# Kernel optimization log

Hardware: AMD Instinct MI355X
Metric: run time of the kernel (lower is better)

Reference implementation:

```python
import jax, jax.numpy as jnp
import numpy as np

B, S, E, H, F = 8, 1024, 1024, 16, 4096
HD = E // H
EPS = 1e-12
NEG = -1e30  # stands in for -inf on fully-masked key positions


def layernorm(x, w, b):
    mu = jnp.mean(x, axis=-1, keepdims=True)
    var = jnp.mean(jnp.square(x - mu), axis=-1, keepdims=True)
    return (x - mu) * jax.lax.rsqrt(var + EPS) * w + b


def setup_inputs() -> dict:
    key = jax.random.key(0)
    ks = jax.random.split(key, 12)
    s = 0.02
    return {
        "final_hidden_state": jax.random.normal(ks[0], (B, S, E), jnp.float32),
        "attention_mask": jax.random.randint(ks[1], (B, S), 0, 2, jnp.int64),
        "token_type_ids": jax.random.randint(ks[2], (B, S), 0, 2, jnp.int64),
        # MultiheadAttention in/out projections (stored input-major: [in, out])
        "in_proj_w": jax.random.normal(ks[3], (E, 3 * E), jnp.float32) * s,
        "in_proj_b": jnp.zeros((3 * E,), jnp.float32),
        "out_proj_w": jax.random.normal(ks[4], (E, E), jnp.float32) * s,
        "out_proj_b": jnp.zeros((E,), jnp.float32),
        # shared LayerNorm
        "ln_w": jnp.ones((E,), jnp.float32),
        "ln_b": jnp.zeros((E,), jnp.float32),
        # FFN
        "w_in": jax.random.normal(ks[5], (E, F), jnp.float32) * s,
        "b_in": jnp.zeros((F,), jnp.float32),
        "w_out": jax.random.normal(ks[6], (F, E), jnp.float32) * s,
        "b_out": jnp.zeros((E,), jnp.float32),
    }


def reference(final_hidden_state, attention_mask, token_type_ids,
              in_proj_w, in_proj_b, out_proj_w, out_proj_b,
              ln_w, ln_b, w_in, b_in, w_out, b_out):
    x = final_hidden_state  # [B,S,E]
    am = attention_mask != 0
    # key_padding_mask: True = ignore this key; first position always masked
    question_mask = (token_type_ids == 1) | (~am)
    question_mask = question_mask.at[:, 0].set(True)  # [B,S]
    # float attn_mask ADDED to scores (PyTorch adds float attn_mask): pairwise 0/1
    amf = (am[:, :, None] & am[:, None, :]).astype(x.dtype)  # [B,S,S]

    # qkv projections
    qkv = x @ in_proj_w + in_proj_b  # [B,S,3E]
    q, k, v = jnp.split(qkv, 3, axis=-1)
    q = q.reshape(B, S, H, HD)
    k = k.reshape(B, S, H, HD)
    v = v.reshape(B, S, H, HD)

    scores = jnp.einsum("bqhd,bkhd->bhqk", q, k) / np.sqrt(HD)
    scores = scores + amf[:, None, :, :]  # additive float mask (0/1!)
    scores = jnp.where(question_mask[:, None, None, :], NEG, scores)
    probs = jax.nn.softmax(scores, axis=-1)

    ctx = jnp.einsum("bhqk,bkhd->bqhd", probs, v).reshape(B, S, E)
    attn_out = ctx @ out_proj_w + out_proj_b

    h = layernorm(attn_out + x, ln_w, ln_b)
    ff = jax.nn.gelu(h @ w_in + b_in, approximate=False) @ w_out + b_out
    return layernorm(ff + h, ln_w, ln_b)
```

## Files before the change

### kernel.cpp

```cpp
#include <hip/hip_runtime.h>
#include <hip/hip_bf16.h>
#include <math.h>

#define B_ 8
#define S_ 1024
#define E_ 1024
#define H_ 16
#define HD_ 64
#define F_ 4096
#define M_ (B_ * S_)

typedef float f32x4 __attribute__((ext_vector_type(4)));
typedef short short8 __attribute__((ext_vector_type(8)));

__device__ inline unsigned short f2bf(float x) {
    union { float f; unsigned int u; } v; v.f = x;
    unsigned int r = (v.u + 0x7fffu + ((v.u >> 16) & 1u)) >> 16;
    return (unsigned short)r;
}
__device__ inline float bf2f(unsigned short u) {
    union { unsigned int u; float f; } v; v.u = ((unsigned int)u) << 16;
    return v.f;
}

__device__ inline float erf_inline(float x) {
    float ax = __builtin_fabsf(x);
    float t = __builtin_amdgcn_rcpf(1.0f + 0.3275911f * ax);
    float y = t * (0.254829592f + t * (-0.284496736f + t * (1.421413741f +
              t * (-1.453152027f + t * 1.061405429f))));
    float e = __expf(-ax * ax);
    float r = 1.0f - y * e;
    union { float f; unsigned int u; } s, o;
    s.f = x; o.f = r;
    o.u = (o.u & 0x7fffffffu) | (s.u & 0x80000000u);
    return o.f;
}

#define AS1 __attribute__((address_space(1)))
#define AS3 __attribute__((address_space(3)))
__device__ inline void gload_lds16(const void* g, void* l) {
    __builtin_amdgcn_global_load_lds((const AS1 unsigned int*)(g),
                                     (AS3 unsigned int*)(l), 16, 0, 0);
}

__global__ __launch_bounds__(256) void cast_f32_bf16(const float* __restrict__ in,
                                                     unsigned short* __restrict__ out) {
    int i = (blockIdx.x * 256 + threadIdx.x) * 4;
    float4 v = *(const float4*)(in + i);
    ushort4 o;
    o.x = f2bf(v.x); o.y = f2bf(v.y); o.z = f2bf(v.z); o.w = f2bf(v.w);
    *(ushort4*)(out + i) = o;
}

__global__ __launch_bounds__(256) void mask_prep(const int* __restrict__ am,
                                                 const int* __restrict__ tt,
                                                 float* __restrict__ amqf,
                                                 float* __restrict__ negadd) {
    int i = blockIdx.x * 256 + threadIdx.x;
    int s = i & (S_ - 1);
    int a = am[i], t = tt[i];
    amqf[i] = (a != 0) ? 1.0f : 0.0f;
    negadd[i] = ((t == 1) || (a == 0) || (s == 0)) ? -1e30f : 0.0f;
}

__global__ __launch_bounds__(256) void transpose_cast(const float* __restrict__ in,
                                                      unsigned short* __restrict__ out,
                                                      int K, int N) {
    __shared__ float tile[32][33];
    int n0 = blockIdx.x * 32, k0 = blockIdx.y * 32;
    int tc = threadIdx.x & 31, tr = threadIdx.x >> 5;
    for (int i = 0; i < 4; ++i) {
        int k = k0 + tr + i * 8;
        tile[tr + i * 8][tc] = in[(size_t)k * N + n0 + tc];
    }
    __syncthreads();
    for (int i = 0; i < 4; ++i) {
        int n = n0 + tr + i * 8;
        out[(size_t)n * K + k0 + tc] = f2bf(tile[tc][tr + i * 8]);
    }
}

#define BM 128
#define BN 128
#define BK 32
template <int EPI>
__global__ __launch_bounds__(256) void gemm_bt(const unsigned short* __restrict__ A,
                                               const unsigned short* __restrict__ Bt,
                                               const float* __restrict__ bias,
                                               const float* __restrict__ res,
                                               unsigned short* __restrict__ Cb,
                                               float* __restrict__ Cf,
                                               int M, int N, int K) {
    __shared__ unsigned short lA[BM * BK];
    __shared__ unsigned short lB[BN * BK];
    int row0 = blockIdx.y * BM, col0 = blockIdx.x * BN;
    int t = threadIdx.x;
    int lane = t & 63, w = t >> 6;
    int wr = w >> 1, wc = w & 1;
    int qa = lane >> 4, ml = lane & 15;

    f32x4 acc[4][4] = {};
    const unsigned short* Aptr = A + (size_t)row0 * K;
    const unsigned short* Bptr = Bt + (size_t)col0 * K;

    for (int k0 = 0; k0 < K; k0 += BK) {
        __syncthreads();
        for (int i = 0; i < 2; ++i) {
            int c = t + i * 256;
            int r = c >> 2, kc = c & 3;
            gload_lds16(Aptr + (size_t)r * K + k0 + kc * 8, lA + c * 8);
            gload_lds16(Bptr + (size_t)r * K + k0 + kc * 8, lB + c * 8);
        }
        __syncthreads();
        short8 af[4], bfr[4];
        for (int i = 0; i < 4; ++i)
            af[i] = *(const short8*)&lA[(wr * 64 + i * 16 + ml) * BK + qa * 8];
        for (int j = 0; j < 4; ++j)
            bfr[j] = *(const short8*)&lB[(wc * 64 + j * 16 + ml) * BK + qa * 8];
        for (int i = 0; i < 4; ++i)
            for (int j = 0; j < 4; ++j)
                acc[i][j] = __builtin_amdgcn_mfma_f32_16x16x32_bf16(af[i], bfr[j], acc[i][j], 0, 0, 0);
    }

    for (int i = 0; i < 4; ++i) {
        for (int j = 0; j < 4; ++j) {
            int col = col0 + wc * 64 + j * 16 + ml;
            float bv = bias[col];
            for (int r = 0; r < 4; ++r) {
                int row = row0 + wr * 64 + i * 16 + qa * 4 + r;
                float cv = acc[i][j][r] + bv;
                if (EPI == 0) {
                    if (col < 1024) cv *= 0.125f;
                    Cb[(size_t)row * N + col] = f2bf(cv);
                } else if (EPI == 1) {
                    cv = 0.5f * cv * (1.0f + erf_inline(cv * 0.70710678118654752f));
                    Cb[(size_t)row * N + col] = f2bf(cv);
                } else {
                    cv += res[(size_t)row * N + col];
                    Cf[(size_t)row * N + col] = cv;
                }
            }
        }
    }
}

__global__ __launch_bounds__(256) void transpose_v(const unsigned short* __restrict__ qkv,
                                                   unsigned short* __restrict__ vT) {
    __shared__ unsigned short tile[64][72];
    int s0 = blockIdx.x * 64;
    int pair = blockIdx.y;
    int b = pair >> 4, h = pair & 15;
    int t = threadIdx.x;
    int r = t >> 2, c0 = (t & 3) * 16;
    const unsigned short* src = qkv + (size_t)(b * S_ + s0 + r) * 3072 + 2048 + h * 64 + c0;
    *(short8*)&tile[r][c0] = *(const short8*)src;
    *(short8*)&tile[r][c0 + 8] = *(const short8*)(src + 8);
    __syncthreads();
    int d = t >> 2, sc0 = (t & 3) * 16;
    unsigned short tmp[16];
    for (int i = 0; i < 16; ++i) tmp[i] = tile[sc0 + i][d];
    unsigned short* dst = vT + ((size_t)pair * 64 + d) * S_ + s0 + sc0;
    *(short8*)dst = *(const short8*)&tmp[0];
    *(short8*)(dst + 8) = *(const short8*)&tmp[8];
}

__global__ __launch_bounds__(256) void attn_flash(const unsigned short* __restrict__ qkv,
                                                  const unsigned short* __restrict__ vT,
                                                  const float* __restrict__ amqf,
                                                  const float* __restrict__ negadd,
                                                  unsigned short* __restrict__ ctx) {
    __shared__ unsigned short lK[128 * 64];
    __shared__ unsigned short lP[4][16 * 136];
    int qc = blockIdx.x;
    int pair = blockIdx.y;
    int b = pair >> 4, h = pair & 15;
    int t = threadIdx.x, w = t >> 6, lane = t & 63;
    int qa = lane >> 4, ml = lane & 15;
    int q0 = qc * 64 + w * 16;

    const unsigned short* qrow = qkv + (size_t)(b * S_ + q0 + ml) * 3072 + h * 64;
    short8 aq0 = *(const short8*)(qrow + qa * 8);
    short8 aq1 = *(const short8*)(qrow + 32 + qa * 8);
    float amq[4];
    for (int r = 0; r < 4; ++r) amq[r] = amqf[b * S_ + q0 + qa * 4 + r];

    const unsigned short* ksrc[4];
    unsigned short* kdst[4];
    for (int i = 0; i < 4; ++i) {
        int c = w * 256 + i * 64 + lane;
        int row = c >> 3, slot = c & 7, e8 = slot ^ (row & 7);
        ksrc[i] = qkv + (size_t)(b * S_ + row) * 3072 + 1024 + h * 64 + e8 * 8;
        kdst[i] = lK + c * 8;
    }
    int sw0 = qa ^ (ml & 7);
    int sw1 = (qa + 4) ^ (ml & 7);

    float m_old[4] = {-3e38f, -3e38f, -3e38f, -3e38f};
    float l[4] = {0.f, 0.f, 0.f, 0.f};
    f32x4 O[4] = {};
    unsigned short* pw = lP[w];

    for (int kc = 0; kc < 8; ++kc) {
        int kk0 = kc * 128;
        __syncthreads();
        for (int i = 0; i < 4; ++i)
            gload_lds16(ksrc[i] + (size_t)kk0 * 3072, kdst[i]);
        __syncthreads();

        f32x4 sacc[8];
        for (int ks = 0; ks < 8; ++ks) {
            int keyoff = (ks * 16 + ml) * 64;
            short8 bb0 = *(const short8*)(lK + keyoff + sw0 * 8);
            short8 bb1 = *(const short8*)(lK + keyoff + sw1 * 8);
            f32x4 a = {};
            a = __builtin_amdgcn_mfma_f32_16x16x32_bf16(aq0, bb0, a, 0, 0, 0);
            a = __builtin_amdgcn_mfma_f32_16x16x32_bf16(aq1, bb1, a, 0, 0, 0);
            float sb = negadd[b * S_ + kk0 + ks * 16 + ml];
            for (int r = 0; r < 4; ++r) a[r] += amq[r] + sb;
            sacc[ks] = a;
        }
        float m_new[4], alpha[4], sum[4];
        for (int r = 0; r < 4; ++r) {
            float m = m_old[r];
            for (int ks = 0; ks < 8; ++ks) m = fmaxf(m, sacc[ks][r]);
            for (int o = 8; o >= 1; o >>= 1) m = fmaxf(m, __shfl_xor(m, o, 16));
            m_new[r] = m;
            alpha[r] = __expf(m_old[r] - m);
            m_old[r] = m;
            sum[r] = 0.f;
        }
        for (int ks = 0; ks < 8; ++ks) {
            for (int r = 0; r < 4; ++r) {
                float p = __expf(sacc[ks][r] - m_new[r]);
                sum[r] += p;
                pw[(qa * 4 + r) * 136 + ks * 16 + ml] = f2bf(p);
            }
        }
        for (int r = 0; r < 4; ++r) {
            float s = sum[r];
            for (int o = 8; o >= 1; o >>= 1) s += __shfl_xor(s, o, 16);
            l[r] = l[r] * alpha[r] + s;
        }
        for (int ds = 0; ds < 4; ++ds)
            for (int r = 0; r < 4; ++r)
                O[ds][r] *= alpha[r];
        for (int ds = 0; ds < 4; ++ds) {
            const unsigned short* vtp = vT + ((size_t)pair * 64 + ds * 16 + ml) * S_ + kk0;
            for (int kst = 0; kst < 4; ++kst) {
                short8 ap = *(const short8*)(pw + ml * 136 + kst * 32 + qa * 8);
                short8 bp = *(const short8*)(vtp + kst * 32 + qa * 8);
                O[ds] = __builtin_amdgcn_mfma_f32_16x16x32_bf16(ap, bp, O[ds], 0, 0, 0);
            }
        }
    }
    for (int r = 0; r < 4; ++r) {
        float inv = 1.0f / l[r];
        size_t orow = (size_t)(b * S_ + q0 + qa * 4 + r) * E_ + h * 64;
        for (int ds = 0; ds < 4; ++ds)
            ctx[orow + ds * 16 + ml] = f2bf(O[ds][r] * inv);
    }
}

template <int WRITE_BF16>
__global__ __launch_bounds__(256) void ln_kernel(const float* __restrict__ in,
                                                 const float* __restrict__ lw,
                                                 const float* __restrict__ lb,
                                                 float* __restrict__ outf,
                                                 unsigned short* __restrict__ outb) {
    int row = blockIdx.x;
    int t = threadIdx.x;
    const float* x = in + (size_t)row * E_;
    float4 v = ((const float4*)x)[t];
    float s = v.x + v.y + v.z + v.w;
    float sq = v.x * v.x + v.y * v.y + v.z * v.z + v.w * v.w;
    for (int o = 32; o >= 1; o >>= 1) {
        s += __shfl_xor(s, o, 64);
        sq += __shfl_xor(sq, o, 64);
    }
    __shared__ float red[8];
    if ((t & 63) == 0) { red[t >> 6] = s; red[4 + (t >> 6)] = sq; }
    __syncthreads();
    s = red[0] + red[1] + red[2] + red[3];
    sq = red[4] + red[5] + red[6] + red[7];
    float mu = s * (1.0f / E_);
    float var = sq * (1.0f / E_) - mu * mu;
    float rstd = rsqrtf(fmaxf(var, 0.0f) + 1e-12f);
    float4 wv = ((const float4*)lw)[t];
    float4 bv = ((const float4*)lb)[t];
    float4 o;
    o.x = (v.x - mu) * rstd * wv.x + bv.x;
    o.y = (v.y - mu) * rstd * wv.y + bv.y;
    o.z = (v.z - mu) * rstd * wv.z + bv.z;
    o.w = (v.w - mu) * rstd * wv.w + bv.w;
    ((float4*)(outf + (size_t)row * E_))[t] = o;
    if (WRITE_BF16) {
        ushort4 ob;
        ob.x = f2bf(o.x); ob.y = f2bf(o.y); ob.z = f2bf(o.z); ob.w = f2bf(o.w);
        ((ushort4*)(outb + (size_t)row * E_))[t] = ob;
    }
}

extern "C" void kernel_launch(void* const* d_in, const int* in_sizes, int n_in,
                              void* d_out, int out_size, void* d_ws, size_t ws_size,
                              hipStream_t stream) {
    const float* x        = (const float*)d_in[0];
    const int*   am       = (const int*)d_in[1];
    const int*   tt       = (const int*)d_in[2];
    const float* in_w     = (const float*)d_in[3];
    const float* in_b     = (const float*)d_in[4];
    const float* out_w    = (const float*)d_in[5];
    const float* out_b    = (const float*)d_in[6];
    const float* ln_w     = (const float*)d_in[7];
    const float* ln_b     = (const float*)d_in[8];
    const float* w_in     = (const float*)d_in[9];
    const float* b_in     = (const float*)d_in[10];
    const float* w_out    = (const float*)d_in[11];
    const float* b_out    = (const float*)d_in[12];
    float* out = (float*)d_out;

    const size_t MB = 1024 * 1024;
    char* ws = (char*)d_ws;
    unsigned short* xb    = (unsigned short*)(ws + 0);
    unsigned short* hb    = xb;
    unsigned short* wqkvT = (unsigned short*)(ws + 16 * MB);
    unsigned short* woutT = (unsigned short*)(ws + 22 * MB);
    unsigned short* winT  = (unsigned short*)(ws + 24 * MB);
    unsigned short* wo2T  = (unsigned short*)(ws + 32 * MB);
    unsigned short* qkvb  = (unsigned short*)(ws + 40 * MB);
    unsigned short* vT    = (unsigned short*)(ws + 88 * MB);
    unsigned short* ctx   = (unsigned short*)(ws + 104 * MB);
    float*          res1  = (float*)(ws + 120 * MB);
    float*          hbuf  = (float*)(ws + 152 * MB);
    unsigned short* ffmid = (unsigned short*)(ws + 184 * MB);
    float*          amqf  = (float*)(ws + 184 * MB);
    float*          negadd= (float*)(ws + 185 * MB);

    cast_f32_bf16<<<dim3(M_ * E_ / 1024), 256, 0, stream>>>(x, xb);
    mask_prep<<<dim3(M_ / 256), 256, 0, stream>>>(am, tt, amqf, negadd);
    transpose_cast<<<dim3(3 * E_ / 32, E_ / 32), 256, 0, stream>>>(in_w, wqkvT, E_, 3 * E_);
    transpose_cast<<<dim3(E_ / 32, E_ / 32), 256, 0, stream>>>(out_w, woutT, E_, E_);
    transpose_cast<<<dim3(F_ / 32, E_ / 32), 256, 0, stream>>>(w_in, winT, E_, F_);
    transpose_cast<<<dim3(E_ / 32, F_ / 32), 256, 0, stream>>>(w_out, wo2T, F_, E_);
    gemm_bt<0><<<dim3(3 * E_ / BN, M_ / BM), 256, 0, stream>>>(xb, wqkvT, in_b, nullptr,
                                                               qkvb, nullptr, M_, 3 * E_, E_);
    transpose_v<<<dim3(S_ / 64, B_ * H_), 256, 0, stream>>>(qkvb, vT);
    attn_flash<<<dim3(S_ / 64, B_ * H_), 256, 0, stream>>>(qkvb, vT, amqf, negadd, ctx);
    gemm_bt<2><<<dim3(E_ / BN, M_ / BM), 256, 0, stream>>>(ctx, woutT, out_b, x,
                                                           nullptr, res1, M_, E_, E_);
    ln_kernel<1><<<dim3(M_), 256, 0, stream>>>(res1, ln_w, ln_b, hbuf, hb);
    gemm_bt<1><<<dim3(F_ / BN, M_ / BM), 256, 0, stream>>>(hb, winT, b_in, nullptr,
                                                           ffmid, nullptr, M_, F_, E_);
    gemm_bt<2><<<dim3(E_ / BN, M_ / BM), 256, 0, stream>>>(ffmid, wo2T, b_out, hbuf,
                                                           nullptr, res1, M_, E_, F_);
    ln_kernel<0><<<dim3(M_), 256, 0, stream>>>(res1, ln_w, ln_b, out, nullptr);
}
```

Baseline: 690.7 us.

## Compute transposed S tile and keep P in registers, dropping LDS round trip

The QK^T MFMA now runs with the K and Q operands swapped, so each lane holds scores for a single query row across keys. The row max and row sum then reduce with two cross-lane shuffles instead of four per row. The P fragments are packed to bf16 with v_cvt_pk_bf16_f32 and rearranged into the PV A-operand layout through lane shuffles, removing the per-warp LDS buffer and its writes and reads. In exchange, alpha and l must be redistributed to the output layout with extra shuffles, and the permutation logic is intricate and easy to get wrong.

```diff
diff --git a/kernel.cpp b/kernel.cpp
--- a/kernel.cpp
+++ b/kernel.cpp
@@ -170,7 +170,6 @@
                                                   const float* __restrict__ negadd,
                                                   unsigned short* __restrict__ ctx) {
     __shared__ unsigned short lK[128 * 64];
-    __shared__ unsigned short lP[4][16 * 136];
     int qc = blockIdx.x;
     int pair = blockIdx.y;
     int b = pair >> 4, h = pair & 15;
@@ -179,10 +178,10 @@
     int q0 = qc * 64 + w * 16;
 
     const unsigned short* qrow = qkv + (size_t)(b * S_ + q0 + ml) * 3072 + h * 64;
-    short8 aq0 = *(const short8*)(qrow + qa * 8);
-    short8 aq1 = *(const short8*)(qrow + 32 + qa * 8);
-    float amq[4];
-    for (int r = 0; r < 4; ++r) amq[r] = amqf[b * S_ + q0 + qa * 4 + r];
+    short8 bq0 = *(const short8*)(qrow + qa * 8);
+    short8 bq1 = *(const short8*)(qrow + 32 + qa * 8);
+    float amq = amqf[b * S_ + q0 + ml];
+    const f32x4* na4 = (const f32x4*)(negadd + b * S_);
 
     const unsigned short* ksrc[4];
     unsigned short* kdst[4];
@@ -194,11 +193,14 @@
     }
     int sw0 = qa ^ (ml & 7);
     int sw1 = (qa + 4) ^ (ml & 7);
-
-    float m_old[4] = {-3e38f, -3e38f, -3e38f, -3e38f};
-    float l[4] = {0.f, 0.f, 0.f, 0.f};
+    int qa4 = qa * 4;
+    int gbase = lane & 48;
+    bool hi = lane >= 32;
+    bool odd = (qa & 1);
+
+    float m_old = -3e38f;
+    float l = 0.f;
     f32x4 O[4] = {};
-    unsigned short* pw = lP[w];
 
     for (int kc = 0; kc < 8; ++kc) {
         int kk0 = kc * 128;
@@ -210,52 +212,78 @@
         f32x4 sacc[8];
         for (int ks = 0; ks < 8; ++ks) {
             int keyoff = (ks * 16 + ml) * 64;
-            short8 bb0 = *(const short8*)(lK + keyoff + sw0 * 8);
-            short8 bb1 = *(const short8*)(lK + keyoff + sw1 * 8);
+            short8 ak0 = *(const short8*)(lK + keyoff + sw0 * 8);
+            short8 ak1 = *(const short8*)(lK + keyoff + sw1 * 8);
             f32x4 a = {};
-            a = __builtin_amdgcn_mfma_f32_16x16x32_bf16(aq0, bb0, a, 0, 0, 0);
-            a = __builtin_amdgcn_mfma_f32_16x16x32_bf16(aq1, bb1, a, 0, 0, 0);
-            float sb = negadd[b * S_ + kk0 + ks * 16 + ml];
-            for (int r = 0; r < 4; ++r) a[r] += amq[r] + sb;
+            a = __builtin_amdgcn_mfma_f32_16x16x32_bf16(ak0, bq0, a, 0, 0, 0);
+            a = __builtin_amdgcn_mfma_f32_16x16x32_bf16(ak1, bq1, a, 0, 0, 0);
+            f32x4 nb = na4[(kk0 >> 2) + ks * 4 + qa];
+            for (int r = 0; r < 4; ++r) a[r] += amq + nb[r];
             sacc[ks] = a;
         }
-        float m_new[4], alpha[4], sum[4];
-        for (int r = 0; r < 4; ++r) {
-            float m = m_old[r];
-            for (int ks = 0; ks < 8; ++ks) m = fmaxf(m, sacc[ks][r]);
-            for (int o = 8; o >= 1; o >>= 1) m = fmaxf(m, __shfl_xor(m, o, 16));
-            m_new[r] = m;
-            alpha[r] = __expf(m_old[r] - m);
-            m_old[r] = m;
-            sum[r] = 0.f;
-        }
-        for (int ks = 0; ks < 8; ++ks) {
+
+        float m = m_old;
+        for (int ks = 0; ks < 8; ++ks)
+            for (int r = 0; r < 4; ++r) m = fmaxf(m, sacc[ks][r]);
+        m = fmaxf(m, __shfl_xor(m, 16));
+        m = fmaxf(m, __shfl_xor(m, 32));
+        float m_new = m;
+        float alpha = __expf(m_old - m_new);
+        m_old = m_new;
+
+        float s_sum = 0.f;
+        short8 pfrag[4];
+        for (int kst = 0; kst < 4; ++kst) {
+            f32x4 e0, e1;
             for (int r = 0; r < 4; ++r) {
-                float p = __expf(sacc[ks][r] - m_new[r]);
-                sum[r] += p;
-                pw[(qa * 4 + r) * 136 + ks * 16 + ml] = f2bf(p);
+                e0[r] = __expf(sacc[2 * kst][r] - m_new);
+                e1[r] = __expf(sacc[2 * kst + 1][r] - m_new);
+                s_sum += e0[r] + e1[r];
             }
-        }
-        for (int r = 0; r < 4; ++r) {
-            float s = sum[r];
-            for (int o = 8; o >= 1; o >>= 1) s += __shfl_xor(s, o, 16);
-            l[r] = l[r] * alpha[r] + s;
-        }
+            unsigned int u0, u1, v0, v1;
+            asm("v_cvt_pk_bf16_f32 %0, %1, %2" : "=v"(u0) : "v"(e0[0]), "v"(e0[1]));
+            asm("v_cvt_pk_bf16_f32 %0, %1, %2" : "=v"(u1) : "v"(e0[2]), "v"(e0[3]));
+            asm("v_cvt_pk_bf16_f32 %0, %1, %2" : "=v"(v0) : "v"(e1[0]), "v"(e1[1]));
+            asm("v_cvt_pk_bf16_f32 %0, %1, %2" : "=v"(v1) : "v"(e1[2]), "v"(e1[3]));
+            unsigned int u0x = __shfl_xor(u0, 32), v0x = __shfl_xor(v0, 32);
+            unsigned int u1x = __shfl_xor(u1, 32), v1x = __shfl_xor(v1, 32);
+            unsigned int A0 = hi ? v0x : u0;
+            unsigned int B0 = hi ? v0  : u0x;
+            unsigned int A1 = hi ? v1x : u1;
+            unsigned int B1 = hi ? v1  : u1x;
+            unsigned int A0x = __shfl_xor(A0, 16), B0x = __shfl_xor(B0, 16);
+            unsigned int A1x = __shfl_xor(A1, 16), B1x = __shfl_xor(B1, 16);
+            union { short8 s8; unsigned int u[4]; } pk;
+            pk.u[0] = odd ? B0x : A0;
+            pk.u[1] = odd ? B1x : A1;
+            pk.u[2] = odd ? B0  : A0x;
+            pk.u[3] = odd ? B1  : A1x;
+            pfrag[kst] = pk.s8;
+        }
+
+        s_sum += __shfl_xor(s_sum, 16);
+        s_sum += __shfl_xor(s_sum, 32);
+        l = l * alpha + s_sum;
+
+        float alf[4];
+        for (int r = 0; r < 4; ++r)
+            alf[r] = __shfl(alpha, gbase | (qa4 + r));
         for (int ds = 0; ds < 4; ++ds)
             for (int r = 0; r < 4; ++r)
-                O[ds][r] *= alpha[r];
+                O[ds][r] *= alf[r];
+
         for (int ds = 0; ds < 4; ++ds) {
             const unsigned short* vtp = vT + ((size_t)pair * 64 + ds * 16 + ml) * S_ + kk0;
             for (int kst = 0; kst < 4; ++kst) {
-                short8 ap = *(const short8*)(pw + ml * 136 + kst * 32 + qa * 8);
                 short8 bp = *(const short8*)(vtp + kst * 32 + qa * 8);
-                O[ds] = __builtin_amdgcn_mfma_f32_16x16x32_bf16(ap, bp, O[ds], 0, 0, 0);
+                O[ds] = __builtin_amdgcn_mfma_f32_16x16x32_bf16(pfrag[kst], bp, O[ds], 0, 0, 0);
             }
         }
     }
     for (int r = 0; r < 4; ++r) {
-        float inv = 1.0f / l[r];
-        size_t orow = (size_t)(b * S_ + q0 + qa * 4 + r) * E_ + h * 64;
+        float lr = __shfl(l, gbase | (qa4 + r));
+        float inv = 1.0f / lr;
+        size_t orow = (size_t)(b * S_ + q0 + qa4 + r) * E_ + h * 64;
         for (int ds = 0; ds < 4; ++ds)
             ctx[orow + ds * 16 + ml] = f2bf(O[ds][r] * inv);
     }
```

New measurement: 866.1 us. 1.25x slower.
